# Kernel tuning notes

Measured on AMD Instinct MI355X. Metric: run time of the kernel, lower is better.

The kernel has to match this reference:

```python
import jax, jax.numpy as jnp
import numpy as np

NUM_HEADS = 8
LN_EPS = 1e-5


def _ln(x, g, b):
    mu = x.mean(-1, keepdims=True)
    xc = x - mu
    v = (xc * xc).mean(-1, keepdims=True)
    return xc * jax.lax.rsqrt(v + LN_EPS) * g + b


def setup_inputs() -> dict:
    key = jax.random.key(0)
    B, T, D, NI, NT = 16, 512, 256, 85, 77
    L, FF, TH = 2, 1024, 32
    ks = iter(jax.random.split(key, 40))
    def nrm(shape, std):
        return jax.random.normal(next(ks), shape, jnp.float32) * std
    inp = {
        'img_tokens': nrm((B, NI, D), 1.0),
        'text_tokens': nrm((B, NT, D), 1.0),
        'task_tokens': nrm((T, D), 0.02),
        'type_task': nrm((D,), 0.02),
        'type_img': nrm((D,), 0.02),
        'type_txt': nrm((D,), 0.02),
        'in_ln_g': jnp.ones((D,), jnp.float32), 'in_ln_b': jnp.zeros((D,), jnp.float32),
        'Wqkv': nrm((L, 3 * D, D), 1.0 / np.sqrt(D)), 'bqkv': jnp.zeros((L, 3 * D), jnp.float32),
        'Wo': nrm((L, D, D), 1.0 / np.sqrt(D)), 'bo': jnp.zeros((L, D), jnp.float32),
        'ln1_g': jnp.ones((L, D), jnp.float32), 'ln1_b': jnp.zeros((L, D), jnp.float32),
        'ln2_g': jnp.ones((L, D), jnp.float32), 'ln2_b': jnp.zeros((L, D), jnp.float32),
        'W1': nrm((L, FF, D), 1.0 / np.sqrt(D)), 'b1': jnp.zeros((L, FF), jnp.float32),
        'W2': nrm((L, D, FF), 1.0 / np.sqrt(FF)), 'b2': jnp.zeros((L, D), jnp.float32),
        'out_ln_g': jnp.ones((D,), jnp.float32), 'out_ln_b': jnp.zeros((D,), jnp.float32),
        'tw1': nrm((T, TH, D), 1.0 / np.sqrt(D)), 'tb1': jnp.zeros((T, TH), jnp.float32),
        'tw2': nrm((T, TH), 1.0 / np.sqrt(TH)), 'tb2': jnp.zeros((T,), jnp.float32),
        'text_mask': jnp.arange(NT)[None, :] < jax.random.randint(next(ks), (B, 1), 10, NT + 1),
        'labels': jax.random.randint(next(ks), (B, T), -1, 2),
    }
    return inp


def reference(img_tokens, text_tokens, task_tokens, type_task, type_img, type_txt,
              in_ln_g, in_ln_b, Wqkv, bqkv, Wo, bo, ln1_g, ln1_b, ln2_g, ln2_b,
              W1, b1, W2, b2, out_ln_g, out_ln_b, tw1, tb1, tw2, tb2,
              text_mask, labels):
    B, NI, D = img_tokens.shape
    T = task_tokens.shape[0]
    L = Wqkv.shape[0]
    hd = D // NUM_HEADS
    available = labels != -1                                   # (B, T)
    n_avail = available.sum(axis=1)                            # (B,)
    # Route B: stable-sort available task ids to the front (permutation per row)
    order = jnp.argsort((~available).astype(jnp.int32), axis=1, stable=True)  # (B, T)
    task_toks = task_tokens[order] + type_task                 # (B, T, D)
    seq = jnp.concatenate([task_toks, img_tokens + type_img, text_tokens + type_txt], axis=1)
    seq = _ln(seq, in_ln_g, in_ln_b)
    task_pad = jnp.arange(T)[None, :] >= n_avail[:, None]
    pad = jnp.concatenate([task_pad, jnp.zeros((B, NI), bool), ~text_mask], axis=1)
    bias = jnp.where(pad, -1e9, 0.0).astype(seq.dtype)[:, None, None, :]  # key-padding mask
    scale = 1.0 / np.sqrt(hd)
    S = seq.shape[1]
    for l in range(L):  # pre-LN transformer encoder layers (eval mode)
        h = _ln(seq, ln1_g[l], ln1_b[l])
        qkv = h @ Wqkv[l].T + bqkv[l]
        q, k, v = jnp.split(qkv, 3, axis=-1)
        q = q.reshape(B, S, NUM_HEADS, hd)
        k = k.reshape(B, S, NUM_HEADS, hd)
        v = v.reshape(B, S, NUM_HEADS, hd)
        scores = jnp.einsum('bqhd,bkhd->bhqk', q, k) * scale + bias
        attn = jax.nn.softmax(scores, axis=-1)
        o = jnp.einsum('bhqk,bkhd->bqhd', attn, v).reshape(B, S, D)
        seq = seq + o @ Wo[l].T + bo[l]
        h2 = _ln(seq, ln2_g[l], ln2_b[l])
        seq = seq + jax.nn.gelu(h2 @ W1[l].T + b1[l], approximate=False) @ W2[l].T + b2[l]
    task_out = _ln(seq[:, :T], out_ln_g, out_ln_b)             # (B, T, D)
    # undo the per-row permutation so task t's token sits at column t, then
    # apply all per-task towers as one grouped matmul (MoE dispatch/combine)
    y = jnp.zeros_like(task_out).at[jnp.arange(B)[:, None], order].set(task_out)
    hsz = jax.nn.relu(jnp.einsum('btd,thd->bth', y, tw1) + tb1[None])
    out = jnp.einsum('bth,th->bt', hsz, tw2) + tb2[None]
    return jnp.where(available, out, jnp.zeros((), out.dtype))
```

## Files before the change

### kernel.cpp

```cpp
#include <hip/hip_runtime.h>
#include <hip/hip_bf16.h>
#include <math.h>

constexpr int B_  = 16;
constexpr int T_  = 512;
constexpr int D_  = 256;
constexpr int NI_ = 85;
constexpr int NT_ = 77;
constexpr int S_  = T_ + NI_ + NT_;
constexpr int M_  = B_ * S_;
constexpr int FF_ = 1024;
constexpr int TH_ = 32;
constexpr int NH_ = 8;
constexpr int KT_ = 704;
constexpr int NKT_ = KT_ / 64;

constexpr float MASK_NEG = -30000.0f;

constexpr int N_FT = 26;
constexpr int OFF_[N_FT + 1] = {
    0,
    348160,
    663552,
    794624,
    794880,
    795136,
    795392,
    795648,
    795904,
    1189120,
    1190656,
    1321728,
    1322240,
    1322752,
    1323264,
    1323776,
    1324288,
    1848576,
    1850624,
    2374912,
    2375424,
    2375680,
    2375936,
    6570240,
    6586624,
    6603008,
    6603520
};
constexpr int TOTAL_ELEMS = OFF_[N_FT];
constexpr int CONV_BLOCKS = (TOTAL_ELEMS + 511) / 512;

typedef __attribute__((ext_vector_type(8))) short bfrag;
typedef __attribute__((ext_vector_type(4))) float f32x4;

__device__ inline float bf2f(__hip_bfloat16 x) { return __bfloat162float(x); }
__device__ inline __hip_bfloat16 f2bf(float x) { return __float2bfloat16(x); }
__device__ inline float wsum64(float v) {
    #pragma unroll
    for (int m = 32; m >= 1; m >>= 1) v += __shfl_xor(v, m, 64);
    return v;
}
__device__ inline bool is_f32_mode(const void* ln_g_raw) {
    return (*(const unsigned int*)ln_g_raw) == 0x3F800000u;
}

__device__ inline bool tile_dead(int m0, int m1, const int* __restrict__ n_avail) {
    int b = m0 / S_;
    int base = b * S_;
    return (m0 >= base + n_avail[b]) && (m1 <= base + T_);
}

__device__ inline void gload_lds16(const __hip_bfloat16* g, __hip_bfloat16* l) {
#if defined(__has_builtin) && __has_builtin(__builtin_amdgcn_global_load_lds)
    __builtin_amdgcn_global_load_lds(
        (const __attribute__((address_space(1))) unsigned int*)g,
        (__attribute__((address_space(3))) unsigned int*)l, 16, 0, 0);
#else
    *reinterpret_cast<uint4*>(l) = *reinterpret_cast<const uint4*>(g);
#endif
}

__device__ inline float gelu_f(float v) {
    return 0.5f * v * (1.f + erff(v * 0.70710678118654752f));
}

struct Ptrs { const void* p[N_FT]; };

__global__ __launch_bounds__(512) void k_init(Ptrs ptrs, __hip_bfloat16* __restrict__ canon,
                                              const int* __restrict__ labels,
                                              int* __restrict__ inv,
                                              int* __restrict__ n_avail) {
    if (blockIdx.x < CONV_BLOCKS) {
        int idx = blockIdx.x * 512 + threadIdx.x;
        if (idx >= TOTAL_ELEMS) return;
        bool f32 = is_f32_mode(ptrs.p[6]);
        int t = 0;
        #pragma unroll
        for (int i = 1; i < N_FT; i++) if (idx >= OFF_[i]) t = i;
        int local = idx - OFF_[t];
        if (f32) canon[idx] = f2bf(((const float*)ptrs.p[t])[local]);
        else     canon[idx] = ((const __hip_bfloat16*)ptrs.p[t])[local];
    } else {
        __shared__ int sc[T_];
        int b = blockIdx.x - CONV_BLOCKS, t = threadIdx.x;
        int av = (labels[b * T_ + t] != -1) ? 1 : 0;
        sc[t] = av;
        __syncthreads();
        for (int off = 1; off < T_; off <<= 1) {
            int v = sc[t];
            int u = (t >= off) ? sc[t - off] : 0;
            __syncthreads();
            sc[t] = v + u;
            __syncthreads();
        }
        int incl  = sc[t];
        int excl  = incl - av;
        int total = sc[T_ - 1];
        inv[b * T_ + t] = av ? excl : (total + (t - excl));
        if (t == 0) n_avail[b] = total;
    }
}

__global__ void k_build(const __hip_bfloat16* __restrict__ img,
                        const __hip_bfloat16* __restrict__ txt,
                        const __hip_bfloat16* __restrict__ task,
                        const __hip_bfloat16* __restrict__ ty_task,
                        const __hip_bfloat16* __restrict__ ty_img,
                        const __hip_bfloat16* __restrict__ ty_txt,
                        const __hip_bfloat16* __restrict__ g,
                        const __hip_bfloat16* __restrict__ bln,
                        const __hip_bfloat16* __restrict__ g1,
                        const __hip_bfloat16* __restrict__ b1,
                        const void* __restrict__ text_mask,
                        const int* __restrict__ inv,
                        const int* __restrict__ n_avail,
                        float* __restrict__ seq,
                        __hip_bfloat16* __restrict__ h1,
                        float* __restrict__ bias) {
    int blk = blockIdx.x;
    int b = blk / S_, j = blk % S_;
    int lane = threadIdx.x;

    int dest;
    float bias_v;
    const __hip_bfloat16* src;
    const __hip_bfloat16* tvec;
    if (j < T_) {
        dest = inv[b * T_ + j];
        src = task + (size_t)j * D_;
        tvec = ty_task;
        bias_v = (dest >= n_avail[b]) ? MASK_NEG : 0.f;
    } else if (j < T_ + NI_) {
        dest = j;
        src = img + (size_t)(b * NI_ + (j - T_)) * D_;
        tvec = ty_img;
        bias_v = 0.f;
    } else {
        int x2 = j - T_ - NI_;
        dest = j;
        src = txt + (size_t)(b * NT_ + x2) * D_;
        tvec = ty_txt;
        const unsigned char* mb = (const unsigned char*)text_mask;
        bool is_byte = (mb[1] != 0);
        int mv = is_byte ? (int)mb[b * NT_ + x2]
                         : ((const int*)text_mask)[b * NT_ + x2];
        bias_v = mv ? 0.f : MASK_NEG;
    }

    float x[4];
    float s = 0.f, ss = 0.f;
    #pragma unroll
    for (int i = 0; i < 4; i++) {
        int d = lane * 4 + i;
        x[i] = bf2f(src[d]) + bf2f(tvec[d]);
        s += x[i];
        ss += x[i] * x[i];
    }
    s = wsum64(s);
    ss = wsum64(ss);
    float mean = s * (1.f / D_);
    float var  = ss * (1.f / D_) - mean * mean;
    float r    = rsqrtf(fmaxf(var, 0.f) + 1e-5f);

    float y[4];
    float s2 = 0.f, ss2 = 0.f;
    float* orow = seq + ((size_t)b * S_ + dest) * D_;
    #pragma unroll
    for (int i = 0; i < 4; i++) {
        int d = lane * 4 + i;
        y[i] = (x[i] - mean) * r * bf2f(g[d]) + bf2f(bln[d]);
        orow[d] = y[i];
        s2 += y[i];
        ss2 += y[i] * y[i];
    }
    s2 = wsum64(s2);
    ss2 = wsum64(ss2);
    float mean2 = s2 * (1.f / D_);
    float var2  = ss2 * (1.f / D_) - mean2 * mean2;
    float r2    = rsqrtf(fmaxf(var2, 0.f) + 1e-5f);
    __hip_bfloat16 tmp[4];
    #pragma unroll
    for (int i = 0; i < 4; i++) {
        int d = lane * 4 + i;
        tmp[i] = f2bf((y[i] - mean2) * r2 * bf2f(g1[d]) + bf2f(b1[d]));
    }
    *reinterpret_cast<uint2*>(h1 + ((size_t)b * S_ + dest) * D_ + lane * 4) =
        *reinterpret_cast<uint2*>(tmp);
    if (lane == 0) bias[b * S_ + dest] = bias_v;
}

template <int GELU>
__global__ __launch_bounds__(256) void k_gemm(const __hip_bfloat16* __restrict__ A,
                                              const __hip_bfloat16* __restrict__ W,
                                              const __hip_bfloat16* __restrict__ bias,
                                              __hip_bfloat16* __restrict__ Cout,
                                              const int* __restrict__ n_avail,
                                              int Mm, int N, int K) {
    constexpr int HALF = 12288;
    __shared__ __align__(16) __hip_bfloat16 Sh[2 * HALF];
    __hip_bfloat16* Es = Sh;

    int m0 = blockIdx.x * 64;
    if (tile_dead(m0, m0 + 64, n_avail)) return;
    int n0 = blockIdx.y * 128;
    int tid = threadIdx.x;
    int w = tid >> 6, lane = tid & 63;
    int lrow = lane & 15, quad = lane >> 4;
    int swz = lrow & 7;

    f32x4 acc[8] = {};

    int kq = (((tid & 7) ^ ((tid >> 3) & 7)) * 8);
    int arow = tid >> 3;
    const __hip_bfloat16* Ar0 = A + (size_t)min(m0 + arow,      Mm - 1) * K + kq;
    const __hip_bfloat16* Ar1 = A + (size_t)min(m0 + arow + 32, Mm - 1) * K + kq;
    const __hip_bfloat16* Wr[4];
    #pragma unroll
    for (int i = 0; i < 4; i++)
        Wr[i] = W + (size_t)(n0 + ((tid + i * 256) >> 3)) * K + kq;

    const int nsteps = K >> 6;

    {
        __hip_bfloat16* As0 = Sh;
        __hip_bfloat16* Ws0 = Sh + 4096;
        gload_lds16(Ar0, As0 + tid * 8);
        gload_lds16(Ar1, As0 + (tid + 256) * 8);
        #pragma unroll
        for (int i = 0; i < 4; i++) gload_lds16(Wr[i], Ws0 + (tid + i * 256) * 8);
    }
    __syncthreads();

    for (int ks = 0; ks < nsteps; ks++) {
        int curo = (ks & 1) * HALF;
        if (ks + 1 < nsteps) {
            int k1 = (ks + 1) << 6;
            __hip_bfloat16* Asn = Sh + (HALF - curo);
            __hip_bfloat16* Wsn = Asn + 4096;
            gload_lds16(Ar0 + k1, Asn + tid * 8);
            gload_lds16(Ar1 + k1, Asn + (tid + 256) * 8);
            #pragma unroll
            for (int i = 0; i < 4; i++) gload_lds16(Wr[i] + k1, Wsn + (tid + i * 256) * 8);
        }
        __hip_bfloat16* Asc = Sh + curo;
        __hip_bfloat16* Wsc = Asc + 4096;
        #pragma unroll
        for (int ko = 0; ko < 2; ko++) {
            int unit = ((ko * 4 + quad) ^ swz) << 3;
            bfrag af = *reinterpret_cast<const bfrag*>(&Asc[(w * 16 + lrow) * 64 + unit]);
            #pragma unroll
            for (int nt = 0; nt < 8; nt++) {
                bfrag bf = *reinterpret_cast<const bfrag*>(&Wsc[(nt * 16 + lrow) * 64 + unit]);
                acc[nt] = __builtin_amdgcn_mfma_f32_16x16x32_bf16(af, bf, acc[nt], 0, 0, 0);
            }
        }
        __syncthreads();
    }

    #pragma unroll
    for (int nt = 0; nt < 8; nt++) {
        int col = nt * 16 + lrow;
        float bv = bf2f(bias[n0 + col]);
        #pragma unroll
        for (int rg = 0; rg < 4; rg++) {
            int row = w * 16 + quad * 4 + rg;
            float v = acc[nt][rg] + bv;
            if (GELU) v = gelu_f(v);
            Es[row * 136 + col] = f2bf(v);
        }
    }
    __syncthreads();

    #pragma unroll
    for (int i = 0; i < 4; i++) {
        int c = tid + i * 256;
        int row = c >> 4, off = (c & 15) * 8;
        int gm = m0 + row;
        if (gm < Mm) {
            uint4 v4 = *reinterpret_cast<const uint4*>(&Es[row * 136 + off]);
            *reinterpret_cast<uint4*>(&Cout[(size_t)gm * N + n0 + off]) = v4;
        }
    }
}

template <int LNOUT>
__global__ __launch_bounds__(256) void k_ffnmega(const __hip_bfloat16* __restrict__ A,
                                                 const __hip_bfloat16* __restrict__ Wop,
                                                 const __hip_bfloat16* __restrict__ bop,
                                                 const __hip_bfloat16* __restrict__ ln2g,
                                                 const __hip_bfloat16* __restrict__ ln2b,
                                                 const __hip_bfloat16* __restrict__ W1p,
                                                 const __hip_bfloat16* __restrict__ b1p,
                                                 const __hip_bfloat16* __restrict__ W2p,
                                                 const __hip_bfloat16* __restrict__ b2p,
                                                 float* __restrict__ seq,
                                                 const __hip_bfloat16* __restrict__ g1n,
                                                 const __hip_bfloat16* __restrict__ b1n,
                                                 __hip_bfloat16* __restrict__ lnout,
                                                 const int* __restrict__ n_avail) {
    constexpr int WST_OFF = 4096;
    constexpr int HT_OFF  = 20480;
    constexpr int ESTRIDE = 260;
    __shared__ __align__(16) __hip_bfloat16 Sh[28672];

    int m0 = blockIdx.x * 32;
    if (tile_dead(m0, m0 + 32, n_avail)) return;
    int tid = threadIdx.x;
    int w = tid >> 6, lane = tid & 63;
    int lrow = lane & 15, quad = lane >> 4;
    int swz = lrow & 7;

    __hip_bfloat16* Pt  = Sh;
    __hip_bfloat16* Wst = Sh + WST_OFF;
    __hip_bfloat16* Ht  = Sh + HT_OFF;

    auto stageW = [&](const __hip_bfloat16* srcbase, int rowstride, __hip_bfloat16* dst) {
        #pragma unroll
        for (int i = 0; i < 4; i++) {
            int u = tid + i * 256;
            int r = u >> 3, c = u & 7;
            gload_lds16(srcbase + (size_t)r * rowstride + ((c ^ (r & 7)) << 3), dst + u * 8);
        }
    };

    #pragma unroll
    for (int i = 0; i < 4; i++) {
        int u = tid + i * 256;
        int r = u >> 5, c = u & 31;
        gload_lds16(A + (size_t)(m0 + r) * 256 + ((c ^ (r & 7)) << 3), Ht + u * 8);
    }
    stageW(Wop, 256, Wst);
    __syncthreads();

    int bufp = 0;
    f32x4 acc[2][4] = {};
    for (int s = 0; s < 8; s++) {
        if (s < 7) {
            int s1 = s + 1;
            stageW(Wop + ((s1 >> 2) * 128) * 256 + (s1 & 3) * 64, 256,
                   Wst + (bufp ^ 1) * 8192);
        }
        int ks = s & 3, h = s >> 2;
        __hip_bfloat16* wb = Wst + bufp * 8192;
        #pragma unroll
        for (int ko = 0; ko < 2; ko++) {
            int aunit = (ks * 8 + ko * 4 + quad) ^ swz;
            int wunit = (ko * 4 + quad) ^ swz;
            bfrag af[2], bf[2];
            #pragma unroll
            for (int mt = 0; mt < 2; mt++)
                af[mt] = *reinterpret_cast<const bfrag*>(&Ht[((mt * 16 + lrow) * 32 + aunit) * 8]);
            #pragma unroll
            for (int nt = 0; nt < 2; nt++)
                bf[nt] = *reinterpret_cast<const bfrag*>(&wb[((w * 32 + nt * 16 + lrow) * 8 + wunit) * 8]);
            #pragma unroll
            for (int mt = 0; mt < 2; mt++)
                #pragma unroll
                for (int nt = 0; nt < 2; nt++)
                    acc[mt][h * 2 + nt] = __builtin_amdgcn_mfma_f32_16x16x32_bf16(af[mt], bf[nt], acc[mt][h * 2 + nt], 0, 0, 0);
        }
        __syncthreads();
        bufp ^= 1;
    }

    float* Es = (float*)Sh;
    #pragma unroll
    for (int j = 0; j < 4; j++) {
        int col = (j >> 1) * 128 + w * 32 + (j & 1) * 16 + lrow;
        float bv = bf2f(bop[col]);
        #pragma unroll
        for (int mt = 0; mt < 2; mt++)
            #pragma unroll
            for (int rg = 0; rg < 4; rg++)
                Es[(mt * 16 + quad * 4 + rg) * ESTRIDE + col] = acc[mt][j][rg] + bv;
    }
    __syncthreads();

    int row = tid >> 3, part = tid & 7;
    size_t gm = (size_t)(m0 + row);
    const float* seqrow = seq + gm * 256 + part * 32;
    float t[32];
    float s = 0.f, ss = 0.f;
    #pragma unroll
    for (int j = 0; j < 8; j++) {
        float4 e  = *reinterpret_cast<const float4*>(&Es[row * ESTRIDE + part * 32 + j * 4]);
        float4 r4 = *reinterpret_cast<const float4*>(&seqrow[j * 4]);
        float v0 = e.x + r4.x, v1 = e.y + r4.y, v2 = e.z + r4.z, v3 = e.w + r4.w;
        t[j * 4 + 0] = v0; t[j * 4 + 1] = v1; t[j * 4 + 2] = v2; t[j * 4 + 3] = v3;
        s += v0 + v1 + v2 + v3;
        ss += v0 * v0 + v1 * v1 + v2 * v2 + v3 * v3;
    }
    #pragma unroll
    for (int mm = 4; mm >= 1; mm >>= 1) {
        s  += __shfl_xor(s,  mm, 8);
        ss += __shfl_xor(ss, mm, 8);
    }
    {
        float mean = s * (1.f / 256);
        float var  = ss * (1.f / 256) - mean * mean;
        float r    = rsqrtf(fmaxf(var, 0.f) + 1e-5f);
        #pragma unroll
        for (int jj = 0; jj < 4; jj++) {
            __hip_bfloat16 hb[8];
            #pragma unroll
            for (int k = 0; k < 8; k++) {
                int col = part * 32 + jj * 8 + k;
                hb[k] = f2bf((t[jj * 8 + k] - mean) * r * bf2f(ln2g[col]) + bf2f(ln2b[col]));
            }
            int unit = (part * 4 + jj) ^ (row & 7);
            *reinterpret_cast<uint4*>(&Ht[row * 256 + unit * 8]) =
                *reinterpret_cast<const uint4*>(hb);
        }
    }
    __syncthreads();
    stageW(W1p, 256, Wst);
    __syncthreads();
    bufp = 0;

    f32x4 acc2[2][4] = {};
    for (int c = 0; c < 8; c++) {
        int ff0 = c << 7;
        f32x4 pacc[2][2] = {};
        for (int ks = 0; ks < 4; ks++) {
            if (ks < 3)
                stageW(W1p + (size_t)ff0 * 256 + (ks + 1) * 64, 256, Wst + (bufp ^ 1) * 8192);
            else
                stageW(W2p + ff0, 1024, Wst + (bufp ^ 1) * 8192);
            __hip_bfloat16* wb = Wst + bufp * 8192;
            #pragma unroll
            for (int ko = 0; ko < 2; ko++) {
                int hunit = (ks * 8 + ko * 4 + quad) ^ swz;
                int wunit = (ko * 4 + quad) ^ swz;
                bfrag af[2], bf[2];
                #pragma unroll
                for (int mt = 0; mt < 2; mt++)
                    af[mt] = *reinterpret_cast<const bfrag*>(&Ht[((mt * 16 + lrow) * 32 + hunit) * 8]);
                #pragma unroll
                for (int nt = 0; nt < 2; nt++)
                    bf[nt] = *reinterpret_cast<const bfrag*>(&wb[((w * 32 + nt * 16 + lrow) * 8 + wunit) * 8]);
                #pragma unroll
                for (int mt = 0; mt < 2; mt++)
                    #pragma unroll
                    for (int nt = 0; nt < 2; nt++)
                        pacc[mt][nt] = __builtin_amdgcn_mfma_f32_16x16x32_bf16(af[mt], bf[nt], pacc[mt][nt], 0, 0, 0);
            }
            if (ks == 3) {
                #pragma unroll
                for (int mt = 0; mt < 2; mt++)
                    #pragma unroll
                    for (int nt = 0; nt < 2; nt++)
                        #pragma unroll
                        for (int rg = 0; rg < 4; rg++) {
                            int prow = mt * 16 + quad * 4 + rg;
                            int pcol = w * 32 + nt * 16 + lrow;
                            float v = pacc[mt][nt][rg] + bf2f(b1p[ff0 + pcol]);
                            v = gelu_f(v);
                            int unit = (pcol >> 3) ^ (prow & 7);
                            Pt[prow * 128 + unit * 8 + (pcol & 7)] = f2bf(v);
                        }
            }
            __syncthreads();
            bufp ^= 1;
        }
        for (int tt = 0; tt < 4; tt++) {
            if (tt < 3) {
                int t1 = tt + 1;
                stageW(W2p + (size_t)((t1 >> 1) * 128) * 1024 + ff0 + (t1 & 1) * 64, 1024,
                       Wst + (bufp ^ 1) * 8192);
            } else if (c < 7) {
                stageW(W1p + (size_t)(ff0 + 128) * 256, 256, Wst + (bufp ^ 1) * 8192);
            }
            int h = tt >> 1, ks2 = tt & 1;
            __hip_bfloat16* wb = Wst + bufp * 8192;
            #pragma unroll
            for (int ko = 0; ko < 2; ko++) {
                int punit = (ks2 * 8 + ko * 4 + quad) ^ swz;
                int wunit = (ko * 4 + quad) ^ swz;
                bfrag af2[2], bf2v[2];
                #pragma unroll
                for (int mt = 0; mt < 2; mt++)
                    af2[mt] = *reinterpret_cast<const bfrag*>(&Pt[((mt * 16 + lrow) * 16 + punit) * 8]);
                #pragma unroll
                for (int nt = 0; nt < 2; nt++)
                    bf2v[nt] = *reinterpret_cast<const bfrag*>(&wb[((w * 32 + nt * 16 + lrow) * 8 + wunit) * 8]);
                #pragma unroll
                for (int mt = 0; mt < 2; mt++)
                    #pragma unroll
                    for (int nt = 0; nt < 2; nt++)
                        acc2[mt][h * 2 + nt] = __builtin_amdgcn_mfma_f32_16x16x32_bf16(af2[mt], bf2v[nt], acc2[mt][h * 2 + nt], 0, 0, 0);
            }
            __syncthreads();
            bufp ^= 1;
        }
    }

    float* Es2 = (float*)Sh;
    #pragma unroll
    for (int j = 0; j < 4; j++) {
        int col = (j >> 1) * 128 + w * 32 + (j & 1) * 16 + lrow;
        float bv = bf2f(b2p[col]);
        #pragma unroll
        for (int mt = 0; mt < 2; mt++)
            #pragma unroll
            for (int rg = 0; rg < 4; rg++)
                Es2[(mt * 16 + quad * 4 + rg) * ESTRIDE + col] = acc2[mt][j][rg] + bv;
    }
    __syncthreads();

    float* seqw = seq + gm * 256 + part * 32;
    float s2 = 0.f, ss2 = 0.f;
    #pragma unroll
    for (int j = 0; j < 8; j++) {
        float4 e = *reinterpret_cast<const float4*>(&Es2[row * ESTRIDE + part * 32 + j * 4]);
        float v0 = t[j * 4 + 0] + e.x, v1 = t[j * 4 + 1] + e.y;
        float v2 = t[j * 4 + 2] + e.z, v3 = t[j * 4 + 3] + e.w;
        t[j * 4 + 0] = v0; t[j * 4 + 1] = v1; t[j * 4 + 2] = v2; t[j * 4 + 3] = v3;
        s2 += v0 + v1 + v2 + v3;
        ss2 += v0 * v0 + v1 * v1 + v2 * v2 + v3 * v3;
        *reinterpret_cast<float4*>(&seqw[j * 4]) = make_float4(v0, v1, v2, v3);
    }
    if (LNOUT) {
        #pragma unroll
        for (int mm = 4; mm >= 1; mm >>= 1) {
            s2  += __shfl_xor(s2,  mm, 8);
            ss2 += __shfl_xor(ss2, mm, 8);
        }
        float mean = s2 * (1.f / 256);
        float var  = ss2 * (1.f / 256) - mean * mean;
        float r    = rsqrtf(fmaxf(var, 0.f) + 1e-5f);
        __hip_bfloat16 ob[32];
        #pragma unroll
        for (int j = 0; j < 32; j++) {
            int col = part * 32 + j;
            ob[j] = f2bf((t[j] - mean) * r * bf2f(g1n[col]) + bf2f(b1n[col]));
        }
        #pragma unroll
        for (int j = 0; j < 4; j++)
            *reinterpret_cast<uint4*>(&lnout[gm * 256 + part * 32 + j * 8]) =
                *reinterpret_cast<const uint4*>(&ob[j * 8]);
    }
}

__global__ __launch_bounds__(256) void k_fattn(const __hip_bfloat16* __restrict__ qkv,
                                               const float* __restrict__ bias,
                                               const int* __restrict__ n_avail,
                                               __hip_bfloat16* __restrict__ out) {
    __shared__ __align__(16) __hip_bfloat16 Vt[2][32 * 72];
    __shared__ __align__(16) __hip_bfloat16 Ps[4][32 * 72];
    __shared__ float Bs[KT_];
    __shared__ int alive[NKT_];
    __shared__ int tlist[NKT_ + 1];
    __shared__ int nact_s;
    int b = blockIdx.z, h = blockIdx.y;
    int q0b = blockIdx.x * 128;
    if (q0b >= n_avail[b] && q0b + 128 <= T_) return;
    int tid = threadIdx.x;
    int wave = tid >> 6, lane = tid & 63;
    int lrow = lane & 15, quad = lane >> 4;
    int q0 = q0b + wave * 32;

    const float scale = 0.17677669529663687f;
    const __hip_bfloat16* base = qkv + (size_t)b * S_ * 768;
    const float* brow = bias + b * S_;

    if (tid < NKT_) alive[tid] = 0;
    __syncthreads();
    for (int i = tid; i < KT_; i += 256) {
        float v = (i < S_) ? brow[i] : MASK_NEG;
        Bs[i] = v;
        if (v != MASK_NEG) alive[i >> 6] = 1;
    }
    __syncthreads();
    if (tid == 0) {
        int n = 0;
        for (int t = 0; t < NKT_; t++) if (alive[t]) tlist[n++] = t;
        if (n == 0) { tlist[0] = 0; n = 1; }
        tlist[n] = tlist[n - 1];
        nact_s = n;
    }
    __syncthreads();
    int nact = nact_s;

    bfrag qf[2];
    {
        int qr0 = min(q0 + lrow, S_ - 1);
        int qr1 = min(q0 + 16 + lrow, S_ - 1);
        qf[0] = *reinterpret_cast<const bfrag*>(base + (size_t)qr0 * 768 + h * 32 + quad * 8);
        qf[1] = *reinterpret_cast<const bfrag*>(base + (size_t)qr1 * 768 + h * 32 + quad * 8);
    }

    bfrag ones_f;
    #pragma unroll
    for (int i = 0; i < 8; i++) ((short*)&ones_f)[i] = (short)0x3F80;

    float m[2][4];
    #pragma unroll
    for (int qh = 0; qh < 2; qh++)
        #pragma unroll
        for (int rg = 0; rg < 4; rg++) m[qh][rg] = -3e38f;
    f32x4 Lacc[2] = {};
    f32x4 O[2][2] = {};

    int skey = lane;
    int sd   = wave * 8;

    bfrag kf_cur[4], vv_cur;
    {
        int k0 = tlist[0] * 64;
        #pragma unroll
        for (int nt = 0; nt < 4; nt++) {
            int kr = min(k0 + nt * 16 + lrow, S_ - 1);
            kf_cur[nt] = *reinterpret_cast<const bfrag*>(base + (size_t)kr * 768 + 256 + h * 32 + quad * 8);
        }
        int kr = min(k0 + skey, S_ - 1);
        vv_cur = *reinterpret_cast<const bfrag*>(base + (size_t)kr * 768 + 512 + h * 32 + sd);
    }

    for (int i = 0; i < nact; i++) {
        int k0 = tlist[i] * 64;
        __hip_bfloat16* vb = Vt[i & 1];

        #pragma unroll
        for (int j = 0; j < 8; j++) vb[(sd + j) * 72 + skey] = ((const __hip_bfloat16*)&vv_cur)[j];
        __syncthreads();

        bfrag kf_nxt[4], vv_nxt;
        {
            int kb = tlist[i + 1] * 64;
            #pragma unroll
            for (int nt = 0; nt < 4; nt++) {
                int kr = min(kb + nt * 16 + lrow, S_ - 1);
                kf_nxt[nt] = *reinterpret_cast<const bfrag*>(base + (size_t)kr * 768 + 256 + h * 32 + quad * 8);
            }
            int kr = min(kb + skey, S_ - 1);
            vv_nxt = *reinterpret_cast<const bfrag*>(base + (size_t)kr * 768 + 512 + h * 32 + sd);
        }

        f32x4 sc[2][4];
        #pragma unroll
        for (int nt = 0; nt < 4; nt++) {
            float bv = Bs[k0 + nt * 16 + lrow];
            #pragma unroll
            for (int qh = 0; qh < 2; qh++) {
                f32x4 z = {};
                sc[qh][nt] = __builtin_amdgcn_mfma_f32_16x16x32_bf16(qf[qh], kf_cur[nt], z, 0, 0, 0);
                #pragma unroll
                for (int rg = 0; rg < 4; rg++) sc[qh][nt][rg] = sc[qh][nt][rg] * scale + bv;
            }
        }

        #pragma unroll
        for (int qh = 0; qh < 2; qh++) {
            float alpha[4];
            #pragma unroll
            for (int rg = 0; rg < 4; rg++) {
                float rm = fmaxf(fmaxf(sc[qh][0][rg], sc[qh][1][rg]), fmaxf(sc[qh][2][rg], sc[qh][3][rg]));
                #pragma unroll
                for (int mm2 = 1; mm2 <= 8; mm2 <<= 1) rm = fmaxf(rm, __shfl_xor(rm, mm2, 64));
                float mn = fmaxf(m[qh][rg], rm);
                alpha[rg] = __expf(m[qh][rg] - mn);
                m[qh][rg] = mn;
                #pragma unroll
                for (int nt = 0; nt < 4; nt++) sc[qh][nt][rg] = __expf(sc[qh][nt][rg] - mn);
            }
            #pragma unroll
            for (int rg = 0; rg < 4; rg++) {
                O[qh][0][rg] *= alpha[rg];
                O[qh][1][rg] *= alpha[rg];
                Lacc[qh][rg] *= alpha[rg];
            }
            #pragma unroll
            for (int nt = 0; nt < 4; nt++)
                #pragma unroll
                for (int rg = 0; rg < 4; rg++)
                    Ps[wave][(qh * 16 + quad * 4 + rg) * 72 + nt * 16 + lrow] = f2bf(sc[qh][nt][rg]);
        }

        #pragma unroll
        for (int qh = 0; qh < 2; qh++) {
            bfrag ap0 = *reinterpret_cast<const bfrag*>(&Ps[wave][(qh * 16 + lrow) * 72 + quad * 8]);
            bfrag ap1 = *reinterpret_cast<const bfrag*>(&Ps[wave][(qh * 16 + lrow) * 72 + 32 + quad * 8]);
            #pragma unroll
            for (int dt = 0; dt < 2; dt++) {
                bfrag bv0 = *reinterpret_cast<const bfrag*>(&vb[(dt * 16 + lrow) * 72 + quad * 8]);
                bfrag bv1 = *reinterpret_cast<const bfrag*>(&vb[(dt * 16 + lrow) * 72 + 32 + quad * 8]);
                O[qh][dt] = __builtin_amdgcn_mfma_f32_16x16x32_bf16(ap0, bv0, O[qh][dt], 0, 0, 0);
                O[qh][dt] = __builtin_amdgcn_mfma_f32_16x16x32_bf16(ap1, bv1, O[qh][dt], 0, 0, 0);
            }
            Lacc[qh] = __builtin_amdgcn_mfma_f32_16x16x32_bf16(ap0, ones_f, Lacc[qh], 0, 0, 0);
            Lacc[qh] = __builtin_amdgcn_mfma_f32_16x16x32_bf16(ap1, ones_f, Lacc[qh], 0, 0, 0);
        }

        #pragma unroll
        for (int nt = 0; nt < 4; nt++) kf_cur[nt] = kf_nxt[nt];
        vv_cur = vv_nxt;
    }

    #pragma unroll
    for (int qh = 0; qh < 2; qh++)
        #pragma unroll
        for (int rg = 0; rg < 4; rg++) {
            int qrow = q0 + qh * 16 + quad * 4 + rg;
            if (qrow < S_) {
                float invl = 1.f / Lacc[qh][rg];
                #pragma unroll
                for (int dt = 0; dt < 2; dt++)
                    out[((size_t)b * S_ + qrow) * D_ + h * 32 + dt * 16 + lrow] = f2bf(O[qh][dt][rg] * invl);
            }
        }
}

__global__ __launch_bounds__(256) void k_final(const float* __restrict__ seq,
                                               const int* __restrict__ inv,
                                               const int* __restrict__ labels,
                                               const __hip_bfloat16* __restrict__ g,
                                               const __hip_bfloat16* __restrict__ bb,
                                               const __hip_bfloat16* __restrict__ tw1,
                                               const __hip_bfloat16* __restrict__ tb1,
                                               const __hip_bfloat16* __restrict__ tw2,
                                               const __hip_bfloat16* __restrict__ tb2,
                                               const void* __restrict__ ln_g_raw,
                                               void* __restrict__ out) {
    int idx = blockIdx.x;
    int t = idx >> 4, b = idx & 15;
    int tid = threadIdx.x;
    bool f32o = is_f32_mode(ln_g_raw);

    int lab = labels[b * T_ + t];
    if (lab == -1) {
        if (tid == 0) {
            if (f32o) ((float*)out)[b * T_ + t] = 0.f;
            else      ((__hip_bfloat16*)out)[b * T_ + t] = f2bf(0.f);
        }
        return;
    }

    __shared__ float y[D_];
    __shared__ float hb[TH_];
    __shared__ float rs[4], rq[4];

    int row = inv[b * T_ + t];
    float x = seq[((size_t)b * S_ + row) * D_ + tid];
    float s1 = wsum64(x);
    float s2 = wsum64(x * x);
    int w = tid >> 6, lane = tid & 63;
    if (lane == 0) { rs[w] = s1; rq[w] = s2; }
    __syncthreads();
    float fs = rs[0] + rs[1] + rs[2] + rs[3];
    float fq = rq[0] + rq[1] + rq[2] + rq[3];
    float mean = fs * (1.f / D_);
    float var  = fq * (1.f / D_) - mean * mean;
    float r    = rsqrtf(fmaxf(var, 0.f) + 1e-5f);
    y[tid] = (x - mean) * r * bf2f(g[tid]) + bf2f(bb[tid]);
    __syncthreads();

    int hh = tid >> 3, part = tid & 7;
    const uint4* w4 = reinterpret_cast<const uint4*>(tw1 + ((size_t)t * TH_ + hh) * D_ + part * 32);
    float acc = 0.f;
    #pragma unroll
    for (int i = 0; i < 4; i++) {
        uint4 kv = w4[i];
        unsigned int wd[4] = {kv.x, kv.y, kv.z, kv.w};
        #pragma unroll
        for (int j2 = 0; j2 < 4; j2++) {
            unsigned int lo = wd[j2] << 16, hi = wd[j2] & 0xffff0000u;
            float flo, fhi;
            __builtin_memcpy(&flo, &lo, 4);
            __builtin_memcpy(&fhi, &hi, 4);
            acc += y[part * 32 + i * 8 + j2 * 2] * flo;
            acc += y[part * 32 + i * 8 + j2 * 2 + 1] * fhi;
        }
    }
    #pragma unroll
    for (int mm = 4; mm >= 1; mm >>= 1) acc += __shfl_down(acc, mm, 8);
    if (part == 0) {
        float hz = acc + bf2f(tb1[t * TH_ + hh]);
        hz = fmaxf(hz, 0.f);
        hb[hh] = hz * bf2f(tw2[t * TH_ + hh]);
    }
    __syncthreads();
    if (tid == 0) {
        float o = bf2f(tb2[t]);
        #pragma unroll
        for (int i = 0; i < TH_; i++) o += hb[i];
        if (f32o) ((float*)out)[b * T_ + t] = o;
        else      ((__hip_bfloat16*)out)[b * T_ + t] = f2bf(o);
    }
}

extern "C" void kernel_launch(void* const* d_in, const int* in_sizes, int n_in,
                              void* d_out, int out_size, void* d_ws, size_t ws_size,
                              hipStream_t stream) {
    const void* tmask  = d_in[26];
    const int*  labels = (const int*)d_in[27];

    char* p = (char*)d_ws;
    auto alloc = [&](size_t bytes) {
        char* r = p;
        p += (bytes + 255) & ~size_t(255);
        return r;
    };
    __hip_bfloat16* canon  = (__hip_bfloat16*)alloc(sizeof(__hip_bfloat16) * (size_t)TOTAL_ELEMS);
    int*            inv     = (int*)alloc(sizeof(int) * B_ * T_);
    int*            n_avail = (int*)alloc(sizeof(int) * B_);
    float*          bias    = (float*)alloc(sizeof(float) * M_);
    float*          seqF    = (float*)alloc(sizeof(float) * (size_t)M_ * D_);
    __hip_bfloat16* bufA    = (__hip_bfloat16*)alloc(sizeof(__hip_bfloat16) * (size_t)M_ * D_);
    __hip_bfloat16* bufBig  = (__hip_bfloat16*)alloc(sizeof(__hip_bfloat16) * (size_t)M_ * FF_);

    Ptrs ptrs;
    for (int i = 0; i < N_FT; i++) ptrs.p[i] = d_in[i];
    hipLaunchKernelGGL(k_init, dim3(CONV_BLOCKS + B_), dim3(512), 0, stream,
                       ptrs, canon, labels, inv, n_avail);

    const __hip_bfloat16* img      = canon + OFF_[0];
    const __hip_bfloat16* txt      = canon + OFF_[1];
    const __hip_bfloat16* task     = canon + OFF_[2];
    const __hip_bfloat16* ty_task  = canon + OFF_[3];
    const __hip_bfloat16* ty_img   = canon + OFF_[4];
    const __hip_bfloat16* ty_txt   = canon + OFF_[5];
    const __hip_bfloat16* in_ln_g  = canon + OFF_[6];
    const __hip_bfloat16* in_ln_b  = canon + OFF_[7];
    const __hip_bfloat16* Wqkv     = canon + OFF_[8];
    const __hip_bfloat16* bqkv     = canon + OFF_[9];
    const __hip_bfloat16* Wo       = canon + OFF_[10];
    const __hip_bfloat16* bo       = canon + OFF_[11];
    const __hip_bfloat16* ln1_g    = canon + OFF_[12];
    const __hip_bfloat16* ln1_b    = canon + OFF_[13];
    const __hip_bfloat16* ln2_g    = canon + OFF_[14];
    const __hip_bfloat16* ln2_b    = canon + OFF_[15];
    const __hip_bfloat16* W1       = canon + OFF_[16];
    const __hip_bfloat16* b1       = canon + OFF_[17];
    const __hip_bfloat16* W2       = canon + OFF_[18];
    const __hip_bfloat16* b2       = canon + OFF_[19];
    const __hip_bfloat16* out_ln_g = canon + OFF_[20];
    const __hip_bfloat16* out_ln_b = canon + OFF_[21];
    const __hip_bfloat16* tw1      = canon + OFF_[22];
    const __hip_bfloat16* tb1      = canon + OFF_[23];
    const __hip_bfloat16* tw2      = canon + OFF_[24];
    const __hip_bfloat16* tb2      = canon + OFF_[25];

    hipLaunchKernelGGL(k_build, dim3(B_ * S_), dim3(64), 0, stream,
                       img, txt, task, ty_task, ty_img, ty_txt, in_ln_g, in_ln_b,
                       ln1_g, ln1_b, tmask, inv, n_avail, seqF, bufA, bias);

    const int mtiles = (M_ + 63) / 64;
    const int rtiles = M_ / 32;
    const int qtiles = (S_ + 127) / 128;

    for (int l = 0; l < 2; l++) {
        hipLaunchKernelGGL((k_gemm<0>), dim3(mtiles, 6), dim3(256), 0, stream,
                           bufA, Wqkv + (size_t)l * 3 * D_ * D_, bqkv + l * 3 * D_,
                           bufBig, n_avail, M_, 3 * D_, D_);
        hipLaunchKernelGGL(k_fattn, dim3(qtiles, NH_, B_), dim3(256), 0, stream,
                           bufBig, bias, n_avail, bufA);
        if (l == 0) {
            hipLaunchKernelGGL((k_ffnmega<1>), dim3(rtiles), dim3(256), 0, stream,
                               bufA,
                               Wo + (size_t)l * D_ * D_, bo + l * D_,
                               ln2_g + l * D_, ln2_b + l * D_,
                               W1 + (size_t)l * FF_ * D_, b1 + l * FF_,
                               W2 + (size_t)l * D_ * FF_, b2 + l * D_,
                               seqF, ln1_g + 1 * D_, ln1_b + 1 * D_, bufA, n_avail);
        } else {
            hipLaunchKernelGGL((k_ffnmega<0>), dim3(rtiles), dim3(256), 0, stream,
                               bufA,
                               Wo + (size_t)l * D_ * D_, bo + l * D_,
                               ln2_g + l * D_, ln2_b + l * D_,
                               W1 + (size_t)l * FF_ * D_, b1 + l * FF_,
                               W2 + (size_t)l * D_ * FF_, b2 + l * D_,
                               seqF, (const __hip_bfloat16*)nullptr,
                               (const __hip_bfloat16*)nullptr,
                               (__hip_bfloat16*)nullptr, n_avail);
        }
    }

    hipLaunchKernelGGL(k_final, dim3(T_ * B_), dim3(256), 0, stream,
                       seqF, inv, labels, out_ln_g, out_ln_b,
                       tw1, tb1, tw2, tb2, d_in[6], d_out);
}
```

Before: 362.8 us.

## Pipeline FFN mega-kernel weight staging with explicit vmcnt waits and flattened loop

The W1/W2 staging loops in the fused FFN kernel become one 64-step loop, and each step's __syncthreads is replaced by a partial s_waitcnt vmcnt plus raw s_barrier and sched_barrier. This lets the next weight tile's global-to-LDS loads stay in flight across the barrier, where the default sync drains them every step. The b1 bias is also cached in shared memory as fp32, removing repeated global loads in the GELU epilogue. The gain relies on hand-counted vmcnt values, which could race if the compiler issues different numbers of memory ops, and the extra LDS may lower occupancy.

Result: slower. 421.6 us (+16.2%).

```diff
diff --git a/kernel.cpp b/kernel.cpp
--- a/kernel.cpp
+++ b/kernel.cpp
@@ -320,8 +320,9 @@
                                                  const int* __restrict__ n_avail) {
     constexpr int WST_OFF = 4096;
     constexpr int HT_OFF  = 20480;
+    constexpr int B1S_OFF = 28672;
     constexpr int ESTRIDE = 260;
-    __shared__ __align__(16) __hip_bfloat16 Sh[28672];
+    __shared__ __align__(16) __hip_bfloat16 Sh[30720];
 
     int m0 = blockIdx.x * 32;
     if (tile_dead(m0, m0 + 32, n_avail)) return;
@@ -333,6 +334,7 @@
     __hip_bfloat16* Pt  = Sh;
     __hip_bfloat16* Wst = Sh + WST_OFF;
     __hip_bfloat16* Ht  = Sh + HT_OFF;
+    float*          b1s = (float*)(Sh + B1S_OFF);
 
     auto stageW = [&](const __hip_bfloat16* srcbase, int rowstride, __hip_bfloat16* dst) {
         #pragma unroll
@@ -343,6 +345,8 @@
         }
     };
 
+    #pragma unroll
+    for (int i = 0; i < 4; i++) b1s[tid + i * 256] = bf2f(b1p[tid + i * 256]);
     #pragma unroll
     for (int i = 0; i < 4; i++) {
         int u = tid + i * 256;
@@ -359,7 +363,12 @@
             int s1 = s + 1;
             stageW(Wop + ((s1 >> 2) * 128) * 256 + (s1 & 3) * 64, 256,
                    Wst + (bufp ^ 1) * 8192);
-        }
+            asm volatile("s_waitcnt vmcnt(4)" ::: "memory");
+        } else {
+            asm volatile("s_waitcnt vmcnt(0)" ::: "memory");
+        }
+        __builtin_amdgcn_s_barrier();
+        __builtin_amdgcn_sched_barrier(0);
         int ks = s & 3, h = s >> 2;
         __hip_bfloat16* wb = Wst + bufp * 8192;
         #pragma unroll
@@ -379,7 +388,9 @@
                 for (int nt = 0; nt < 2; nt++)
                     acc[mt][h * 2 + nt] = __builtin_amdgcn_mfma_f32_16x16x32_bf16(af[mt], bf[nt], acc[mt][h * 2 + nt], 0, 0, 0);
         }
-        __syncthreads();
+        asm volatile("s_waitcnt lgkmcnt(0)" ::: "memory");
+        __builtin_amdgcn_sched_barrier(0);
+        __builtin_amdgcn_s_barrier();
         bufp ^= 1;
     }
 
@@ -438,18 +449,37 @@
     bufp = 0;
 
     f32x4 acc2[2][4] = {};
-    for (int c = 0; c < 8; c++) {
-        int ff0 = c << 7;
-        f32x4 pacc[2][2] = {};
-        for (int ks = 0; ks < 4; ks++) {
-            if (ks < 3)
-                stageW(W1p + (size_t)ff0 * 256 + (ks + 1) * 64, 256, Wst + (bufp ^ 1) * 8192);
-            else
-                stageW(W2p + ff0, 1024, Wst + (bufp ^ 1) * 8192);
-            __hip_bfloat16* wb = Wst + bufp * 8192;
+    f32x4 pacc[2][2] = {};
+    for (int q = 0; q < 64; q++) {
+        int c = q >> 3, r8 = q & 7;
+        if (q < 63) {
+            int q1 = q + 1, c1 = q1 >> 3, r1 = q1 & 7;
+            const __hip_bfloat16* nb;
+            int nstride;
+            if (r1 < 4) { nb = W1p + (size_t)(c1 * 128) * 256 + r1 * 64; nstride = 256; }
+            else { int t1 = r1 - 4;
+                   nb = W2p + (size_t)((t1 >> 1) * 128) * 1024 + c1 * 128 + (t1 & 1) * 64;
+                   nstride = 1024; }
+            stageW(nb, nstride, Wst + (bufp ^ 1) * 8192);
+            asm volatile("s_waitcnt vmcnt(4)" ::: "memory");
+        } else {
+            asm volatile("s_waitcnt vmcnt(0)" ::: "memory");
+        }
+        __builtin_amdgcn_s_barrier();
+        __builtin_amdgcn_sched_barrier(0);
+        __hip_bfloat16* wb = Wst + bufp * 8192;
+        if (r8 < 4) {
+            if (r8 == 0) {
+                #pragma unroll
+                for (int mt = 0; mt < 2; mt++)
+                    #pragma unroll
+                    for (int nt = 0; nt < 2; nt++)
+                        #pragma unroll
+                        for (int e = 0; e < 4; e++) pacc[mt][nt][e] = 0.f;
+            }
             #pragma unroll
             for (int ko = 0; ko < 2; ko++) {
-                int hunit = (ks * 8 + ko * 4 + quad) ^ swz;
+                int hunit = (r8 * 8 + ko * 4 + quad) ^ swz;
                 int wunit = (ko * 4 + quad) ^ swz;
                 bfrag af[2], bf[2];
                 #pragma unroll
@@ -464,7 +494,7 @@
                     for (int nt = 0; nt < 2; nt++)
                         pacc[mt][nt] = __builtin_amdgcn_mfma_f32_16x16x32_bf16(af[mt], bf[nt], pacc[mt][nt], 0, 0, 0);
             }
-            if (ks == 3) {
+            if (r8 == 3) {
                 #pragma unroll
                 for (int mt = 0; mt < 2; mt++)
                     #pragma unroll
@@ -473,25 +503,14 @@
                         for (int rg = 0; rg < 4; rg++) {
                             int prow = mt * 16 + quad * 4 + rg;
                             int pcol = w * 32 + nt * 16 + lrow;
-                            float v = pacc[mt][nt][rg] + bf2f(b1p[ff0 + pcol]);
+                            float v = pacc[mt][nt][rg] + b1s[(c << 7) + pcol];
                             v = gelu_f(v);
                             int unit = (pcol >> 3) ^ (prow & 7);
                             Pt[prow * 128 + unit * 8 + (pcol & 7)] = f2bf(v);
                         }
             }
-            __syncthreads();
-            bufp ^= 1;
-        }
-        for (int tt = 0; tt < 4; tt++) {
-            if (tt < 3) {
-                int t1 = tt + 1;
-                stageW(W2p + (size_t)((t1 >> 1) * 128) * 1024 + ff0 + (t1 & 1) * 64, 1024,
-                       Wst + (bufp ^ 1) * 8192);
-            } else if (c < 7) {
-                stageW(W1p + (size_t)(ff0 + 128) * 256, 256, Wst + (bufp ^ 1) * 8192);
-            }
-            int h = tt >> 1, ks2 = tt & 1;
-            __hip_bfloat16* wb = Wst + bufp * 8192;
+        } else {
+            int tt = r8 - 4, h = tt >> 1, ks2 = tt & 1;
             #pragma unroll
             for (int ko = 0; ko < 2; ko++) {
                 int punit = (ks2 * 8 + ko * 4 + quad) ^ swz;
@@ -509,9 +528,11 @@
                     for (int nt = 0; nt < 2; nt++)
                         acc2[mt][h * 2 + nt] = __builtin_amdgcn_mfma_f32_16x16x32_bf16(af2[mt], bf2v[nt], acc2[mt][h * 2 + nt], 0, 0, 0);
             }
-            __syncthreads();
-            bufp ^= 1;
-        }
+        }
+        asm volatile("s_waitcnt lgkmcnt(0)" ::: "memory");
+        __builtin_amdgcn_sched_barrier(0);
+        __builtin_amdgcn_s_barrier();
+        bufp ^= 1;
     }
 
     float* Es2 = (float*)Sh;
```
